# Kernel optimization log

Hardware: AMD Instinct MI355X
Metric: run time of the kernel (lower is better)

## Reference

```python
import jax, jax.numpy as jnp
import numpy as np


def setup_inputs() -> dict:
    key = jax.random.key(0)
    ks = jax.random.split(key, 24)
    B, S = 64, 4096
    E, C, N = 64, 32, 16          # Event_num, Categorical_num, Numerical_num
    EMB, HS, EF, DIM = 128, 256, 128, 64
    u = lambda k, sh: jax.random.uniform(k, sh, jnp.float32, -1.0, 1.0)
    return {
        "event": jax.random.normal(ks[0], (B, S, E), jnp.float32),
        "time": jax.random.normal(ks[1], (B, S, 1), jnp.float32),
        "vc": jax.random.normal(ks[2], (B, S, C), jnp.float32),
        "vn": jax.random.normal(ks[3], (B, S, N), jnp.float32),
        "h0": jax.random.normal(ks[4], (B, HS), jnp.float32),
        "c0": jax.random.normal(ks[5], (B, HS), jnp.float32),
        "Wx": u(ks[6], (EMB, 4 * HS)),
        "Wh": u(ks[7], (HS, 4 * HS)),
        "Wc": u(ks[8], (3, HS)),
        "bias": u(ks[9], (4 * HS,)),
        "Ve": u(ks[10], (E, EMB)),
        "Vc": u(ks[11], (C, EMB)),
        "Vn": u(ks[12], (N, EMB)),
        "Wlin": u(ks[13], (HS, DIM)),   # nn.Linear stored as [in, out]
        "blin": u(ks[14], (DIM,)),
        "Wef1": u(ks[15], (EMB, EF)),
        "bef1": u(ks[16], (EF,)),
        "Wef3": u(ks[17], (EF, HS)),
        "bef3": u(ks[18], (HS,)),
    }


def reference(event, time, vc, vn, h0, c0, Wx, Wh, Wc, bias, Ve, Vc, Vn,
              Wlin, blin, Wef1, bef1, Wef3, bef3):
    HS = Wh.shape[0]
    # Batched (time-independent) projections, computed once for all steps.
    s = jnp.einsum("bse,eh->bsh", event, Ve)                       # [B,S,EMB]
    x = s + 2.0 * (jnp.einsum("bsc,ch->bsh", vc, Vc)
                   + jnp.tanh(jnp.einsum("bsn,nh->bsh", vn, Vn)))  # [B,S,EMB]
    xW = jnp.einsum("bsh,hg->bsg", x, Wx)                          # [B,S,4HS]
    # event-filter gate j_t, also time-independent
    j = jax.nn.sigmoid(jnp.tanh(s @ Wef1 + bef1) @ Wef3 + bef3)    # [B,S,HS]

    def step(carry, inp):
        h, c = carry
        xw_t, j_t = inp
        gates = xw_t + h @ Wh + bias
        i_t = jax.nn.sigmoid(gates[:, :HS] + c * Wc[0])
        f_t = jax.nn.sigmoid(gates[:, HS:2 * HS] + c * Wc[1])
        g_t = jnp.tanh(gates[:, 2 * HS:3 * HS])
        o_t = jax.nn.sigmoid(gates[:, 3 * HS:] + c * Wc[2])
        c_hat = f_t * c + i_t * g_t
        c_new = j_t * c_hat + (1.0 - j_t) * c
        h_hat = o_t * jnp.tanh(c_hat)
        h_new = j_t * h_hat + (1.0 - j_t) * h
        return (h_new, c_new), None

    (h_t, _), _ = jax.lax.scan(step, (h0, c0),
                               (jnp.swapaxes(xW, 0, 1), jnp.swapaxes(j, 0, 1)))
    return h_t @ Wlin + blin
```

## Files before the change

### kernel.cpp

```cpp
#include <hip/hip_runtime.h>
#include <cstdint>
#include <cstddef>

typedef __attribute__((ext_vector_type(8))) short bf16x8;
typedef __attribute__((ext_vector_type(4))) float f32x4;
typedef uint16_t u16;
typedef uint32_t u32;
typedef uint64_t u64;

#define NS 4096

#define OFF_HX4    ((size_t)0)
#define OFF_HXM    ((size_t)262144)
#define OFF_STATE  ((size_t)524288)
#define OFF_WHT    ((size_t)655360)
#define OFF_WXTH   (OFF_WHT   + (size_t)524288)
#define OFF_WXTL   (OFF_WXTH  + (size_t)262144)
#define OFF_WEF1H  (OFF_WXTL  + (size_t)262144)
#define OFF_WEF1L  (OFF_WEF1H + (size_t)32768)
#define OFF_WEF3H  (OFF_WEF1L + (size_t)32768)
#define OFF_WEF3L  (OFF_WEF3H + (size_t)65536)
#define OFF_CH     ((size_t)2*1024*1024)
#define CH_BYTES_PER_SC ((size_t)425984)

static __device__ __forceinline__ float bf2f(u16 u){
  union { uint32_t i; float f; } v; v.i = ((uint32_t)u) << 16; return v.f;
}
static __device__ __forceinline__ u16 f2bf(float f){
  union { float f; uint32_t u; } v; v.f = f;
  uint32_t r = v.u + 0x7fffu + ((v.u >> 16) & 1u);
  return (u16)(r >> 16);
}
static __device__ __forceinline__ float sigmoid_f(float x){
  return 1.f / (1.f + __expf(-x));
}
static __device__ __forceinline__ float tanh_f(float x){
  x = fminf(15.f, fmaxf(-15.f, x));
  float e = __expf(2.f * x);
  return 1.f - 2.f / (e + 1.f);
}
static __device__ __forceinline__ u64 agld64(const u64* p){
  return __hip_atomic_load(p, __ATOMIC_RELAXED, __HIP_MEMORY_SCOPE_AGENT);
}
static __device__ __forceinline__ void agst64(u64* p, u64 v){
  __hip_atomic_store(p, v, __ATOMIC_RELAXED, __HIP_MEMORY_SCOPE_AGENT);
}

__global__ void k_prep(const float* __restrict__ Wh, const float* __restrict__ Wx,
                       const float* __restrict__ Wef1, const float* __restrict__ Wef3,
                       u16* __restrict__ WhT,
                       u16* __restrict__ WxTh, u16* __restrict__ WxTl,
                       u16* __restrict__ Wef1h, u16* __restrict__ Wef1l,
                       u16* __restrict__ Wef3h, u16* __restrict__ Wef3l){
  int idx = blockIdx.x*256 + threadIdx.x;
  if (idx < 262144){ int n = idx>>8, k = idx&255; WhT[idx] = f2bf(Wh[k*1024+n]); return; }
  idx -= 262144;
  if (idx < 131072){
    int n = idx>>7, k = idx&127; float w = Wx[k*1024+n];
    u16 h = f2bf(w); WxTh[idx] = h; WxTl[idx] = f2bf(w - bf2f(h)); return;
  }
  idx -= 131072;
  if (idx < 16384){
    int n = idx>>7, k = idx&127; float w = Wef1[k*128+n];
    u16 h = f2bf(w); Wef1h[idx] = h; Wef1l[idx] = f2bf(w - bf2f(h)); return;
  }
  idx -= 16384;
  if (idx < 32768){
    int n = idx>>7, k = idx&127; float w = Wef3[k*256+n];
    u16 h = f2bf(w); Wef3h[idx] = h; Wef3l[idx] = f2bf(w - bf2f(h)); return;
  }
}

__global__ void k_seed(const float* __restrict__ h0, u64* __restrict__ hX4,
                       u64* __restrict__ hXM){
  int idx = blockIdx.x*256 + threadIdx.x;
  int gr = idx >> 7, p = idx & 127;
  u16 he = f2bf(h0[(size_t)gr*256 + 2*p]);
  u16 ho = f2bf(h0[(size_t)gr*256 + 2*p + 1]);
  int g = gr >> 4, r = gr & 15;
  u64 v = (u64)he | ((u64)ho << 16);
  size_t o = (size_t)(3*4 + g)*2048 + p*16 + r;
  hX4[o] = v; hXM[o] = v;
}

__global__ __launch_bounds__(256) void k_embed(
    const float* __restrict__ event, const float* __restrict__ vc, const float* __restrict__ vn,
    const float* __restrict__ Ve, const float* __restrict__ Vc, const float* __restrict__ Vn,
    u16* __restrict__ sHi, u16* __restrict__ sLo,
    u16* __restrict__ xHi, u16* __restrict__ xLo, int c0){
  __shared__ float VeL[64*128];
  __shared__ float VcL[32*128];
  __shared__ float VnL[16*128];
  __shared__ float evL[16*64];
  __shared__ float vcL[16*32];
  __shared__ float vnL[16*16];
  const int tid = threadIdx.x;
  const int sc = blockIdx.x >> 2;
  const int b0 = (blockIdx.x & 3) * 16;
  const int ss = c0 + sc;
  for (int i = tid; i < 64*128; i += 256) VeL[i] = Ve[i];
  for (int i = tid; i < 32*128; i += 256) VcL[i] = Vc[i];
  for (int i = tid; i < 16*128; i += 256) VnL[i] = Vn[i];
  for (int i = tid; i < 16*64; i += 256)
    evL[i] = event[((size_t)(b0 + (i>>6))*4096 + ss)*64 + (i&63)];
  for (int i = tid; i < 16*32; i += 256)
    vcL[i] = vc[((size_t)(b0 + (i>>5))*4096 + ss)*32 + (i&31)];
  for (int i = tid; i < 16*16; i += 256)
    vnL[i] = vn[((size_t)(b0 + (i>>4))*4096 + ss)*16 + (i&15)];
  __syncthreads();
  const int n = tid & 127, half = tid >> 7;
  for (int r = half; r < 16; r += 2){
    float sd = 0.f, cd = 0.f, nd = 0.f;
    #pragma unroll 8
    for (int k = 0; k < 64; ++k) sd = fmaf(evL[r*64+k], VeL[k*128+n], sd);
    #pragma unroll 8
    for (int k = 0; k < 32; ++k) cd = fmaf(vcL[r*32+k], VcL[k*128+n], cd);
    #pragma unroll 8
    for (int k = 0; k < 16; ++k) nd = fmaf(vnL[r*16+k], VnL[k*128+n], nd);
    float x = sd + 2.f*(cd + tanh_f(nd));
    size_t o = ((size_t)sc*64 + b0 + r)*128 + n;
    u16 sh = f2bf(sd); sHi[o] = sh; sLo[o] = f2bf(sd - bf2f(sh));
    u16 xh = f2bf(x);  xHi[o] = xh; xLo[o] = f2bf(x  - bf2f(xh));
  }
}

template<int ACT, int OUTKIND, int NTILES>
__global__ __launch_bounds__(256) void k_gemm(
    const u16* __restrict__ Ahi, const u16* __restrict__ Alo,
    const u16* __restrict__ BTh, const u16* __restrict__ BTl,
    const float* __restrict__ bias,
    float* __restrict__ CoutF, u16* __restrict__ CoutHi, u16* __restrict__ CoutLo){
  __shared__ u16 aLh[4][16*136];
  __shared__ u16 aLl[4][16*136];
  const int tid = threadIdx.x, lane = tid & 63, w = tid >> 6;
  const int c15 = lane & 15, q4 = lane >> 4;
  const size_t mbase = (size_t)blockIdx.x*64 + (size_t)w*16;
  const u16* Aph = Ahi + mbase*128;
  const u16* Apl = Alo + mbase*128;
  #pragma unroll
  for (int i = 0; i < 4; ++i){
    int row = q4 + i*4;
    *(bf16x8*)(&aLh[w][row*136 + c15*8]) = *(const bf16x8*)(Aph + row*128 + c15*8);
    *(bf16x8*)(&aLl[w][row*136 + c15*8]) = *(const bf16x8*)(Apl + row*128 + c15*8);
  }
  __syncthreads();
  bf16x8 ah[4], al[4];
  #pragma unroll
  for (int q = 0; q < 4; ++q){
    ah[q] = *(const bf16x8*)(&aLh[w][c15*136 + q*32 + q4*8]);
    al[q] = *(const bf16x8*)(&aLl[w][c15*136 + q*32 + q4*8]);
  }
  const u16* Bph = BTh + c15*128 + q4*8;
  const u16* Bpl = BTl + c15*128 + q4*8;

  bf16x8 bh[4], bl[4], bhn[4], bln[4];
  #pragma unroll
  for (int q = 0; q < 4; ++q){ bh[q] = *(const bf16x8*)(Bph + q*32); bl[q] = *(const bf16x8*)(Bpl + q*32); }

  for (int nt = 0; nt < NTILES; ++nt){
    if (nt + 1 < NTILES){
      #pragma unroll
      for (int q = 0; q < 4; ++q){
        bhn[q] = *(const bf16x8*)(Bph + (nt+1)*2048 + q*32);
        bln[q] = *(const bf16x8*)(Bpl + (nt+1)*2048 + q*32);
      }
    }
    f32x4 acc = (f32x4){0.f,0.f,0.f,0.f};
    #pragma unroll
    for (int q = 0; q < 4; ++q){
      acc = __builtin_amdgcn_mfma_f32_16x16x32_bf16(al[q], bh[q], acc, 0, 0, 0);
      acc = __builtin_amdgcn_mfma_f32_16x16x32_bf16(ah[q], bl[q], acc, 0, 0, 0);
      acc = __builtin_amdgcn_mfma_f32_16x16x32_bf16(ah[q], bh[q], acc, 0, 0, 0);
    }
    const int n = nt*16 + c15;
    const float bv = bias[n];
    #pragma unroll
    for (int i = 0; i < 4; ++i){
      float v = acc[i] + bv;
      if (ACT == 1) v = tanh_f(v);
      else if (ACT == 2) v = sigmoid_f(v);
      const size_t m = mbase + q4*4 + i;
      if (OUTKIND == 0){
        CoutF[m*(size_t)(NTILES*16) + n] = v;
      } else if (OUTKIND == 1){
        CoutF[m*1024 + (size_t)(n & 255)*4 + (size_t)(n >> 8)] = v;
      } else {
        size_t o = m*(size_t)(NTILES*16) + n;
        u16 hh = f2bf(v); CoutHi[o] = hh; CoutLo[o] = f2bf(v - bf2f(hh));
      }
    }
    #pragma unroll
    for (int q = 0; q < 4; ++q){ bh[q] = bhn[q]; bl[q] = bln[q]; }
  }
}

__global__ __launch_bounds__(256, 1) void k_scan(
    const u16* __restrict__ WhT, const float* __restrict__ xwG, const float* __restrict__ jG,
    const float* __restrict__ Wc, const float* __restrict__ h0, const float* __restrict__ c0in,
    const float* __restrict__ Wlin, const float* __restrict__ blin,
    u64* __restrict__ hX4, u64* __restrict__ hXM, float* __restrict__ stateF,
    float* __restrict__ out, int T0, int SC, int FINAL)
{
  const int xcd  = blockIdx.x & 7;
  const int ring = blockIdx.x >> 3;
  if (xcd >= 4) return;
  const int g = xcd, s = ring;

  const int tid  = threadIdx.x;
  const int lane = tid & 63;
  const int w    = tid >> 6;
  const int c15  = lane & 15;
  const int q4   = lane >> 4;
  const int ghid = s*64 + w*16 + c15;
  const int FIRST = (T0 == 0);

  bf16x8 Bf[4][8];
  {
    const u16* bp = WhT + (size_t)ghid*256 + q4*8;
    #pragma unroll
    for (int gt = 0; gt < 4; ++gt)
      #pragma unroll
      for (int q = 0; q < 8; ++q)
        Bf[gt][q] = *(const bf16x8*)(bp + (size_t)gt*65536 + q*32);
  }

  float creg[4], hreg[4];
  #pragma unroll
  for (int i = 0; i < 4; ++i){
    int r = q4*4 + i;
    if (FIRST){
      creg[i] = c0in[(size_t)(g*16 + r)*256 + ghid];
      hreg[i] = h0[(size_t)(g*16 + r)*256 + ghid];
    } else {
      creg[i] = stateF[(size_t)(g*16 + r)*256 + ghid];
      hreg[i] = stateF[16384 + (size_t)(g*16 + r)*256 + ghid];
    }
  }
  const float wc0 = Wc[ghid], wc1 = Wc[256 + ghid], wc2 = Wc[512 + ghid];

  const int P = s*32 + w*8 + (c15 >> 1);

  f32x4 xqA[4], xqB[4]; float jvA[4], jvB[4];
  auto ldxw = [&](int tn, f32x4* xq, float* jv){
    const float* xwp = xwG + ((size_t)tn*64 + g*16)*1024 + (size_t)ghid*4;
    const float* jp  = jG  + ((size_t)tn*64 + g*16)*256 + ghid;
    #pragma unroll
    for (int i = 0; i < 4; ++i){
      int r = q4*4 + i;
      xq[i] = *(const f32x4*)(xwp + (size_t)r*1024);
      jv[i] = jp[(size_t)r*256];
    }
  };
  ldxw(0, xqA, jvA);

  bool fastOK = true;

  auto step = [&](int t, f32x4* xq, float* jv, f32x4* xqN, float* jvN){
    const unsigned T = (unsigned)(T0 + t);
    const int rb = (int)((T + 3) & 3);
    const int wb = (int)(T & 3);
    const u64* hrL = hX4 + (size_t)(rb*4 + g)*2048 + c15;
    const u64* hrM = hXM + (size_t)(rb*4 + g)*2048 + c15;

    u64 d[8][4];
    bool got = false;
    if (fastOK){
      int it = 0;
      for(;;){
        #pragma unroll
        for (int q = 0; q < 8; ++q)
          #pragma unroll
          for (int jj = 0; jj < 4; ++jj)
            d[q][jj] = __builtin_nontemporal_load(hrL + (q*16 + q4*4 + jj)*16);
        bool ok = true;
        #pragma unroll
        for (int q = 0; q < 8; ++q)
          #pragma unroll
          for (int jj = 0; jj < 4; ++jj)
            ok &= ((u32)(d[q][jj] >> 32) == T);
        if (ok){ got = true; break; }
        if (++it >= 512) break;
        asm volatile("" ::: "memory");
      }
      if (!got) fastOK = false;
    }
    if (!got){
      for(;;){
        #pragma unroll
        for (int q = 0; q < 8; ++q)
          #pragma unroll
          for (int jj = 0; jj < 4; ++jj)
            d[q][jj] = agld64(hrM + (q*16 + q4*4 + jj)*16);
        bool ok = true;
        #pragma unroll
        for (int q = 0; q < 8; ++q)
          #pragma unroll
          for (int jj = 0; jj < 4; ++jj)
            ok &= ((u32)(d[q][jj] >> 32) == T);
        if (ok) break;
      }
    }

    bf16x8 Af[8];
    #pragma unroll
    for (int q = 0; q < 8; ++q){
      union { u32 dd[4]; bf16x8 v; } cv;
      #pragma unroll
      for (int jj = 0; jj < 4; ++jj) cv.dd[jj] = (u32)d[q][jj];
      Af[q] = cv.v;
    }

    if (t + 1 < SC) ldxw(t + 1, xqN, jvN);

    f32x4 acc[4];
    #pragma unroll
    for (int gt = 0; gt < 4; ++gt) acc[gt] = (f32x4){0.f,0.f,0.f,0.f};
    #pragma unroll
    for (int q = 0; q < 8; ++q)
      #pragma unroll
      for (int gt = 0; gt < 4; ++gt)
        acc[gt] = __builtin_amdgcn_mfma_f32_16x16x32_bf16(Af[q], Bf[gt][q], acc[gt], 0, 0, 0);

    u16 hb[4];
    #pragma unroll
    for (int i = 0; i < 4; ++i){
      float ip = acc[0][i] + xq[i][0] + creg[i]*wc0;
      float fp = acc[1][i] + xq[i][1] + creg[i]*wc1;
      float gp = acc[2][i] + xq[i][2];
      float op = acc[3][i] + xq[i][3] + creg[i]*wc2;
      float it2 = sigmoid_f(ip);
      float ft = sigmoid_f(fp);
      float gt = tanh_f(gp);
      float ot = sigmoid_f(op);
      float chat = ft*creg[i] + it2*gt;
      float cn = creg[i] + jv[i]*(chat - creg[i]);
      float hhat = ot*tanh_f(chat);
      float hn = hreg[i] + jv[i]*(hhat - hreg[i]);
      creg[i] = cn; hreg[i] = hn;
      hb[i] = f2bf(hn);
    }

    u32 a = (u32)hb[0] | ((u32)hb[1] << 16);
    u32 b = (u32)hb[2] | ((u32)hb[3] << 16);
    u32 pa = (u32)__shfl_xor((int)a, 1, 64);
    u32 pb = (u32)__shfl_xor((int)b, 1, 64);
    u64* hwL = hX4 + (size_t)(wb*4 + g)*2048 + (size_t)P*16;
    u64* hwM = hXM + (size_t)(wb*4 + g)*2048 + (size_t)P*16;
    const u64 tag = ((u64)(T + 1)) << 32;
    if ((lane & 1) == 0){
      u64 v0 = tag | (u64)((a & 0xffffu) | ((pa & 0xffffu) << 16));
      u64 v1 = tag | (u64)((a >> 16) | (pa & 0xffff0000u));
      hwL[q4*4 + 0] = v0;  hwL[q4*4 + 1] = v1;
      agst64(hwM + q4*4 + 0, v0); agst64(hwM + q4*4 + 1, v1);
    } else {
      u64 v2 = tag | (u64)((pb & 0xffffu) | ((b & 0xffffu) << 16));
      u64 v3 = tag | (u64)((pb >> 16) | (b & 0xffff0000u));
      hwL[q4*4 + 2] = v2;  hwL[q4*4 + 3] = v3;
      agst64(hwM + q4*4 + 2, v2); agst64(hwM + q4*4 + 3, v3);
    }
    asm volatile("" ::: "memory");
  };

  for (int t = 0; t < SC; t += 2){
    step(t,     xqA, jvA, xqB, jvB);
    step(t + 1, xqB, jvB, xqA, jvA);
  }

  if (!FINAL){
    #pragma unroll
    for (int i = 0; i < 4; ++i){
      int r = q4*4 + i;
      stateF[(size_t)(g*16 + r)*256 + ghid] = creg[i];
      stateF[16384 + (size_t)(g*16 + r)*256 + ghid] = hreg[i];
    }
  }

  if (FINAL && s == 0){
    __shared__ float hF[16*256];
    const unsigned tgt = (unsigned)NS;
    for (int idx = tid; idx < 2048; idx += 256){
      int r = idx >> 7, p = idx & 127;
      const u64* ap = hXM + (size_t)(3*4 + g)*2048 + p*16 + r;
      u64 v;
      do { v = agld64(ap); } while ((u32)(v >> 32) != tgt);
      hF[r*256 + 2*p]     = bf2f((u16)v);
      hF[r*256 + 2*p + 1] = bf2f((u16)(v >> 16));
    }
    __syncthreads();
    for (int idx = tid; idx < 1024; idx += 256){
      int r = idx >> 6, dcol = idx & 63;
      float aacc = blin[dcol];
      for (int k = 0; k < 256; ++k)
        aacc = fmaf(hF[r*256 + k], Wlin[k*64 + dcol], aacc);
      out[(size_t)(g*16 + r)*64 + dcol] = aacc;
    }
  }
}

extern "C" void kernel_launch(void* const* d_in, const int* in_sizes, int n_in,
                              void* d_out, int out_size, void* d_ws, size_t ws_size,
                              hipStream_t stream)
{
  (void)in_sizes; (void)n_in;
  const float* event = (const float*)d_in[0];
  const float* vc    = (const float*)d_in[2];
  const float* vn    = (const float*)d_in[3];
  const float* h0    = (const float*)d_in[4];
  const float* c0v   = (const float*)d_in[5];
  const float* Wx    = (const float*)d_in[6];
  const float* Wh    = (const float*)d_in[7];
  const float* Wc    = (const float*)d_in[8];
  const float* bias  = (const float*)d_in[9];
  const float* Ve    = (const float*)d_in[10];
  const float* Vc    = (const float*)d_in[11];
  const float* Vn    = (const float*)d_in[12];
  const float* Wlin  = (const float*)d_in[13];
  const float* blin  = (const float*)d_in[14];
  const float* Wef1  = (const float*)d_in[15];
  const float* bef1  = (const float*)d_in[16];
  const float* Wef3  = (const float*)d_in[17];
  const float* bef3  = (const float*)d_in[18];

  int SC = 0;
  const int cands[9] = {4096, 2048, 1024, 512, 256, 128, 64, 32, 16};
  for (int i = 0; i < 9; ++i){
    if (OFF_CH + (size_t)cands[i]*CH_BYTES_PER_SC <= ws_size){ SC = cands[i]; break; }
  }
  if (SC == 0){
    hipMemsetAsync(d_out, 0, (size_t)out_size*sizeof(float), stream);
    return;
  }
  const int C = NS / SC;

  char* ws = (char*)d_ws;
  u64*   hX4    = (u64*)(ws + OFF_HX4);
  u64*   hXM    = (u64*)(ws + OFF_HXM);
  float* stateF = (float*)(ws + OFF_STATE);
  u16* WhT   = (u16*)(ws + OFF_WHT);
  u16* WxTh  = (u16*)(ws + OFF_WXTH);
  u16* WxTl  = (u16*)(ws + OFF_WXTL);
  u16* Wef1h = (u16*)(ws + OFF_WEF1H);
  u16* Wef1l = (u16*)(ws + OFF_WEF1L);
  u16* Wef3h = (u16*)(ws + OFF_WEF3H);
  u16* Wef3l = (u16*)(ws + OFF_WEF3L);
  char* ch = ws + OFF_CH;
  u16* sHi  = (u16*)ch;
  u16* sLo  = (u16*)(ch + (size_t)SC*16384);
  u16* xHi  = (u16*)(ch + (size_t)SC*32768);
  u16* xLo  = (u16*)(ch + (size_t)SC*49152);
  u16* e1Hi = (u16*)(ch + (size_t)SC*65536);
  u16* e1Lo = (u16*)(ch + (size_t)SC*81920);
  float* xwG = (float*)(ch + (size_t)SC*98304);
  float* jG  = (float*)(ch + (size_t)SC*360448);

  k_prep<<<1728, 256, 0, stream>>>(Wh, Wx, Wef1, Wef3, WhT, WxTh, WxTl,
                                   Wef1h, Wef1l, Wef3h, Wef3l);
  k_seed<<<32, 256, 0, stream>>>(h0, hX4, hXM);

  for (int c = 0; c < C; ++c){
    const int c0 = c * SC;
    k_embed<<<SC*4, 256, 0, stream>>>(event, vc, vn, Ve, Vc, Vn, sHi, sLo, xHi, xLo, c0);
    k_gemm<0,1,64><<<SC, 256, 0, stream>>>(xHi, xLo, WxTh, WxTl, bias, xwG, nullptr, nullptr);
    k_gemm<1,2,8><<<SC, 256, 0, stream>>>(sHi, sLo, Wef1h, Wef1l, bef1, nullptr, e1Hi, e1Lo);
    k_gemm<2,0,16><<<SC, 256, 0, stream>>>(e1Hi, e1Lo, Wef3h, Wef3l, bef3, jG, nullptr, nullptr);
    k_scan<<<32, 256, 0, stream>>>(WhT, xwG, jG, Wc, h0, c0v, Wlin, blin,
                                   hX4, hXM, stateF, (float*)d_out, c0, SC, (c == C-1) ? 1 : 0);
  }
}
```

Before: 15.66 ms.

## Use LDS for block-local h slice and consume remote h regions as they arrive

Each block now keeps its own 64-column slice of the bf16 hidden state in a double-buffered LDS array and runs the MFMAs for that slice right after a __syncthreads, with no global polling. The remaining three regions, written by other blocks, are polled separately and each one's MFMAs run as soon as its tags match, so compute overlaps with waiting for slower producers. The Wh fragments in registers are reordered by rotation to line up with this region order. The cost is a __syncthreads per step, per-region wave-wide votes, a buffer_inv in the spin loop, and more complex control flow.

```diff
diff --git a/kernel.cpp b/kernel.cpp
--- a/kernel.cpp
+++ b/kernel.cpp
@@ -44,6 +44,19 @@
 }
 static __device__ __forceinline__ void agst64(u64* p, u64 v){
   __hip_atomic_store(p, v, __ATOMIC_RELAXED, __HIP_MEMORY_SCOPE_AGENT);
+}
+
+template<int RI>
+static __device__ __forceinline__ void procRegion(f32x4 (&acc)[4], const u64 (&dd)[8],
+                                                  const bf16x8 (&Bf)[4][8]){
+  union { u32 w[4]; bf16x8 v; } c0, c1;
+  #pragma unroll
+  for (int jj = 0; jj < 4; ++jj){ c0.w[jj] = (u32)dd[jj]; c1.w[jj] = (u32)dd[4+jj]; }
+  #pragma unroll
+  for (int gt = 0; gt < 4; ++gt){
+    acc[gt] = __builtin_amdgcn_mfma_f32_16x16x32_bf16(c0.v, Bf[gt][2+2*RI], acc[gt], 0, 0, 0);
+    acc[gt] = __builtin_amdgcn_mfma_f32_16x16x32_bf16(c1.v, Bf[gt][3+2*RI], acc[gt], 0, 0, 0);
+  }
 }
 
 __global__ void k_prep(const float* __restrict__ Wh, const float* __restrict__ Wx,
@@ -214,14 +227,19 @@
   const int ghid = s*64 + w*16 + c15;
   const int FIRST = (T0 == 0);
 
+  __shared__ __align__(16) u16 hOwnL[2][16][72];
+
   bf16x8 Bf[4][8];
   {
     const u16* bp = WhT + (size_t)ghid*256 + q4*8;
     #pragma unroll
     for (int gt = 0; gt < 4; ++gt)
       #pragma unroll
-      for (int q = 0; q < 8; ++q)
-        Bf[gt][q] = *(const bf16x8*)(bp + (size_t)gt*65536 + q*32);
+      for (int rot = 0; rot < 4; ++rot)
+        #pragma unroll
+        for (int half = 0; half < 2; ++half)
+          Bf[gt][rot*2 + half] =
+            *(const bf16x8*)(bp + (size_t)gt*65536 + (size_t)(((s+rot)&3)*64 + half*32));
   }
 
   float creg[4], hreg[4];
@@ -236,6 +254,10 @@
       hreg[i] = stateF[16384 + (size_t)(g*16 + r)*256 + ghid];
     }
   }
+  #pragma unroll
+  for (int i = 0; i < 4; ++i)
+    hOwnL[T0 & 1][q4*4 + i][w*16 + c15] = f2bf(hreg[i]);
+
   const float wc0 = Wc[ghid], wc1 = Wc[256 + ghid], wc2 = Wc[512 + ghid];
 
   const int P = s*32 + w*8 + (c15 >> 1);
@@ -259,67 +281,91 @@
     const unsigned T = (unsigned)(T0 + t);
     const int rb = (int)((T + 3) & 3);
     const int wb = (int)(T & 3);
-    const u64* hrL = hX4 + (size_t)(rb*4 + g)*2048 + c15;
-    const u64* hrM = hXM + (size_t)(rb*4 + g)*2048 + c15;
-
-    u64 d[8][4];
-    bool got = false;
+    const u64* baseL = hX4 + (size_t)(rb*4 + g)*2048;
+    const u64* baseM = hXM + (size_t)(rb*4 + g)*2048;
+
+    __syncthreads();
+
+    f32x4 acc[4];
+    #pragma unroll
+    for (int gt = 0; gt < 4; ++gt) acc[gt] = (f32x4){0.f,0.f,0.f,0.f};
+    {
+      const u16* hop = &hOwnL[T & 1][c15][q4*8];
+      bf16x8 a0 = *(const bf16x8*)(hop);
+      bf16x8 a1 = *(const bf16x8*)(hop + 32);
+      #pragma unroll
+      for (int gt = 0; gt < 4; ++gt){
+        acc[gt] = __builtin_amdgcn_mfma_f32_16x16x32_bf16(a0, Bf[gt][0], acc[gt], 0, 0, 0);
+        acc[gt] = __builtin_amdgcn_mfma_f32_16x16x32_bf16(a1, Bf[gt][1], acc[gt], 0, 0, 0);
+      }
+    }
+
+    u64 dR[3][8];
+    bool need[3] = {true, true, true};
+    int needCnt = 3;
+
     if (fastOK){
       int it = 0;
-      for(;;){
+      while (needCnt && it < 1024){
+        asm volatile("buffer_inv sc0" ::: "memory");
         #pragma unroll
-        for (int q = 0; q < 8; ++q)
+        for (int ri = 0; ri < 3; ++ri){
+          if (need[ri]){
+            const size_t ro = (size_t)((((unsigned)(s+1+ri)) & 3)*512 + q4*64 + c15);
+            #pragma unroll
+            for (int h2 = 0; h2 < 2; ++h2)
+              #pragma unroll
+              for (int jj = 0; jj < 4; ++jj)
+                dR[ri][h2*4+jj] = *((volatile const u64*)(baseL + ro + h2*256 + jj*16));
+          }
+        }
+        #pragma unroll
+        for (int ri = 0; ri < 3; ++ri){
+          if (need[ri]){
+            bool ok = true;
+            #pragma unroll
+            for (int jj = 0; jj < 8; ++jj) ok &= ((u32)(dR[ri][jj] >> 32) == T);
+            if (__all(ok)){
+              need[ri] = false; --needCnt;
+              if (ri == 0)      procRegion<0>(acc, dR[0], Bf);
+              else if (ri == 1) procRegion<1>(acc, dR[1], Bf);
+              else              procRegion<2>(acc, dR[2], Bf);
+            }
+          }
+        }
+        ++it;
+      }
+      if (needCnt) fastOK = false;
+    }
+    while (needCnt){
+      #pragma unroll
+      for (int ri = 0; ri < 3; ++ri){
+        if (need[ri]){
+          const size_t ro = (size_t)((((unsigned)(s+1+ri)) & 3)*512 + q4*64 + c15);
           #pragma unroll
-          for (int jj = 0; jj < 4; ++jj)
-            d[q][jj] = __builtin_nontemporal_load(hrL + (q*16 + q4*4 + jj)*16);
-        bool ok = true;
-        #pragma unroll
-        for (int q = 0; q < 8; ++q)
+          for (int h2 = 0; h2 < 2; ++h2)
+            #pragma unroll
+            for (int jj = 0; jj < 4; ++jj)
+              dR[ri][h2*4+jj] = agld64(baseM + ro + h2*256 + jj*16);
+        }
+      }
+      #pragma unroll
+      for (int ri = 0; ri < 3; ++ri){
+        if (need[ri]){
+          bool ok = true;
           #pragma unroll
-          for (int jj = 0; jj < 4; ++jj)
-            ok &= ((u32)(d[q][jj] >> 32) == T);
-        if (ok){ got = true; break; }
-        if (++it >= 512) break;
-        asm volatile("" ::: "memory");
+          for (int jj = 0; jj < 8; ++jj) ok &= ((u32)(dR[ri][jj] >> 32) == T);
+          if (__all(ok)){
+            need[ri] = false; --needCnt;
+            if (ri == 0)      procRegion<0>(acc, dR[0], Bf);
+            else if (ri == 1) procRegion<1>(acc, dR[1], Bf);
+            else              procRegion<2>(acc, dR[2], Bf);
+          }
+        }
       }
-      if (!got) fastOK = false;
-    }
-    if (!got){
-      for(;;){
-        #pragma unroll
-        for (int q = 0; q < 8; ++q)
-          #pragma unroll
-          for (int jj = 0; jj < 4; ++jj)
-            d[q][jj] = agld64(hrM + (q*16 + q4*4 + jj)*16);
-        bool ok = true;
-        #pragma unroll
-        for (int q = 0; q < 8; ++q)
-          #pragma unroll
-          for (int jj = 0; jj < 4; ++jj)
-            ok &= ((u32)(d[q][jj] >> 32) == T);
-        if (ok) break;
-      }
-    }
-
-    bf16x8 Af[8];
-    #pragma unroll
-    for (int q = 0; q < 8; ++q){
-      union { u32 dd[4]; bf16x8 v; } cv;
-      #pragma unroll
-      for (int jj = 0; jj < 4; ++jj) cv.dd[jj] = (u32)d[q][jj];
-      Af[q] = cv.v;
     }
 
     if (t + 1 < SC) ldxw(t + 1, xqN, jvN);
-
-    f32x4 acc[4];
-    #pragma unroll
-    for (int gt = 0; gt < 4; ++gt) acc[gt] = (f32x4){0.f,0.f,0.f,0.f};
-    #pragma unroll
-    for (int q = 0; q < 8; ++q)
-      #pragma unroll
-      for (int gt = 0; gt < 4; ++gt)
-        acc[gt] = __builtin_amdgcn_mfma_f32_16x16x32_bf16(Af[q], Bf[gt][q], acc[gt], 0, 0, 0);
 
     u16 hb[4];
     #pragma unroll
@@ -339,6 +385,10 @@
       creg[i] = cn; hreg[i] = hn;
       hb[i] = f2bf(hn);
     }
+
+    #pragma unroll
+    for (int i = 0; i < 4; ++i)
+      hOwnL[(T + 1) & 1][q4*4 + i][w*16 + c15] = hb[i];
 
     u32 a = (u32)hb[0] | ((u32)hb[1] << 16);
     u32 b = (u32)hb[2] | ((u32)hb[3] << 16);
```

After: 20.99 ms. 1.34x slower.
